# Kernel optimization log

Hardware: AMD Instinct MI355X
Metric: run time of the kernel (lower is better)

The kernel has to match this reference:

```python
import jax, jax.numpy as jnp
import numpy as np
from jax.scipy.special import logsumexp

D = 256; H = 8; A = D // H
B_CONST = 0.9; P_MAX = 50000.0; P_MIN = 1e-4; TANH_RATE = 0.005; EPS = 1e-10
SCALE = 1.0 / np.sqrt(D)


def setup_inputs() -> dict:
    key = jax.random.key(0)
    ks = jax.random.split(key, 5)
    B, S = 2, 512
    context = jax.random.normal(ks[0], (B, S, D), dtype=jnp.float32)
    W_Q = jax.random.normal(ks[1], (D, D), dtype=jnp.float32) * (1.0 / np.sqrt(D))
    W_KV = jax.random.normal(ks[2], (2 * D, D), dtype=jnp.float32) * (1.0 / np.sqrt(D))
    W_out = jax.random.normal(ks[3], (D, D), dtype=jnp.float32) * (1.0 / np.sqrt(D))
    p_param = jax.random.normal(ks[4], (D,), dtype=jnp.float32) * 0.02
    return {"context": context, "W_Q": W_Q, "W_KV": W_KV, "W_out": W_out, "p_param": p_param}


def reference(context, W_Q, W_KV, W_out, p_param):
    B, S, _ = context.shape
    # projections (nn.Linear: x @ W.T)
    q = context @ W_Q.T                          # [B,S,D]
    kv = context @ W_KV.T                        # [B,S,2D]
    k, v = kv[..., :D], kv[..., D:]
    # scaled p: p_max*tanh(tanh_rate*p)+1, then replace exact zeros with p_min
    p = P_MAX * jnp.tanh(TANH_RATE * p_param) + 1.0
    p = p + (p == 0).astype(p.dtype) * P_MIN
    # minmax-normalize v over the key/sequence axis into [b, 1]
    v_max = jnp.max(v, axis=-2, keepdims=True)   # [B,1,D]
    v_min = jnp.min(v, axis=-2, keepdims=True)
    v = (1.0 - B_CONST) * (v - v_min) / (v_max - v_min + EPS) + B_CONST
    z = p * jnp.log(v)                           # [B,S,D]
    # split heads
    qh = q.reshape(B, S, H, A).transpose(0, 2, 1, 3)          # [B,H,S,A]
    kh = k.reshape(B, S, H, A).transpose(0, 2, 1, 3)          # [B,H,S,A]
    zh = z.reshape(B, S, H, A).transpose(0, 2, 1, 3)[:, :, None]  # [B,H,1,K,A]
    dot = jnp.einsum('bhqa,bhka->bhqk', qh, kh)
    w = jax.nn.log_softmax(dot * SCALE, axis=-1)              # [B,H,Q,K]
    # log-domain power mean: logsumexp over keys of log-weights + p*log(v)
    mean = logsumexp(w[..., None] + zh, axis=-2)              # [B,H,Q,A]
    mean = mean.transpose(0, 2, 1, 3).reshape(B, S, D)
    e = jnp.exp(mean / p)
    # invert v minmax normalization
    e = (e - B_CONST) * (v_max - v_min + EPS) / (1.0 - B_CONST) + v_min
    return e @ W_out.T
```

## Files before the change

kernel.cpp:

```cpp
#include <hip/hip_runtime.h>
#include <math.h>

#define DD 256
#define HH 8
#define AA 32
#define SS 512
#define BB 2
constexpr float BCONST      = 0.9f;
constexpr float ONE_MINUS_B = 0.1f;
constexpr float EPSF        = 1e-10f;
constexpr float SCALEF      = 0.0625f;
constexpr float FLTMAX      = 3.402823466e38f;

#define OFF_QKV    0
#define OFF_VP     786432
#define OFF_EW     1048576
#define OFF_PMIN   1310720
#define OFF_PMAX   1318912
#define OFF_VMIN   1327104
#define OFF_VRANGE 1327616
#define OFF_P      1328128

#define KB4(buf, row, col4) \
  (&(buf)[((row) << 5) | ((((col4) >> 2) ^ (((row) >> 2) & 7)) << 2)])

template<int TM, int TN, int RM, int RN, bool MM>
__global__ __launch_bounds__(256) void gemm_t(
    const float* __restrict__ A, const float* __restrict__ B0,
    const float* __restrict__ B1, int nsplit,
    float* __restrict__ C, int ldc, int K, int lda,
    float* __restrict__ pminP, float* __restrict__ pmaxP) {
  constexpr int LDT = 36;
  constexpr int CG  = TN / RN;
  constexpr int NA  = TM * 32 / 1024;
  constexpr int NB  = TN * 32 / 1024;
  __shared__ float As[TM][LDT];
  __shared__ float Bs[TN][LDT];
  const int i0 = blockIdx.x * TM;
  const int j0 = blockIdx.y * TN;
  const float* Bsrc = (j0 < nsplit) ? (B0 + (size_t)j0 * K)
                                    : (B1 + (size_t)(j0 - nsplit) * K);
  const int t  = threadIdx.x;
  const int lr = t >> 3;
  const int lc = (t & 7) << 2;
  const int tx = t % CG, ty = t / CG;

  float4 pa[NA], pb[NB];
#pragma unroll
  for (int u = 0; u < NA; ++u)
    pa[u] = *(const float4*)(A + (size_t)(i0 + lr + 32 * u) * lda + lc);
#pragma unroll
  for (int u = 0; u < NB; ++u)
    pb[u] = *(const float4*)(Bsrc + (size_t)(lr + 32 * u) * K + lc);

  float acc[RM][RN] = {};
  for (int k0 = 0; k0 < K; k0 += 32) {
    __syncthreads();
#pragma unroll
    for (int u = 0; u < NA; ++u) *(float4*)&As[lr + 32 * u][lc] = pa[u];
#pragma unroll
    for (int u = 0; u < NB; ++u) *(float4*)&Bs[lr + 32 * u][lc] = pb[u];
    __syncthreads();
    if (k0 + 32 < K) {
#pragma unroll
      for (int u = 0; u < NA; ++u)
        pa[u] = *(const float4*)(A + (size_t)(i0 + lr + 32 * u) * lda + k0 + 32 + lc);
#pragma unroll
      for (int u = 0; u < NB; ++u)
        pb[u] = *(const float4*)(Bsrc + (size_t)(lr + 32 * u) * K + k0 + 32 + lc);
    }
#pragma unroll
    for (int kk = 0; kk < 32; kk += 4) {
      float4 af[RM], bf[RN];
#pragma unroll
      for (int r = 0; r < RM; ++r) af[r] = *(const float4*)&As[ty * RM + r][kk];
#pragma unroll
      for (int c = 0; c < RN; ++c) bf[c] = *(const float4*)&Bs[tx + CG * c][kk];
#pragma unroll
      for (int r = 0; r < RM; ++r)
#pragma unroll
        for (int c = 0; c < RN; ++c)
          acc[r][c] += af[r].x * bf[c].x + af[r].y * bf[c].y +
                       af[r].z * bf[c].z + af[r].w * bf[c].w;
    }
  }
#pragma unroll
  for (int r = 0; r < RM; ++r)
#pragma unroll
    for (int c = 0; c < RN; ++c)
      C[(size_t)(i0 + ty * RM + r) * ldc + j0 + tx + CG * c] = acc[r][c];

  if (MM && j0 >= 512) {
    __syncthreads();
    float* mnb = &As[0][0];
    float* mxb = &Bs[0][0];
#pragma unroll
    for (int c = 0; c < RN; ++c) {
      float mn = acc[0][c], mx = acc[0][c];
#pragma unroll
      for (int r = 1; r < RM; ++r) {
        mn = fminf(mn, acc[r][c]);
        mx = fmaxf(mx, acc[r][c]);
      }
      mnb[(tx + CG * c) * 17 + ty] = mn;
      mxb[(tx + CG * c) * 17 + ty] = mx;
    }
    __syncthreads();
    if (t < TN) {
      float mn = mnb[t * 17], mx = mxb[t * 17];
#pragma unroll
      for (int i = 1; i < 16; ++i) {
        mn = fminf(mn, mnb[t * 17 + i]);
        mx = fmaxf(mx, mxb[t * 17 + i]);
      }
      const int bx = i0 >> 5;
      pminP[bx * 256 + (j0 - 512) + t] = mn;
      pmaxP[bx * 256 + (j0 - 512) + t] = mx;
    }
  }
}

__global__ __launch_bounds__(256) void vpk(
    const float* __restrict__ qkv, const float* __restrict__ pminP,
    const float* __restrict__ pmaxP, const float* __restrict__ p_param,
    float* __restrict__ vp, float* __restrict__ vminw,
    float* __restrict__ vrangew, float* __restrict__ pw) {
  const int blk = blockIdx.x;
  const int b = blk >> 9, s = blk & 511;
  const int d = threadIdx.x;
  float mn = pminP[(b * 16) * 256 + d];
  float mx = pmaxP[(b * 16) * 256 + d];
#pragma unroll
  for (int c = 1; c < 16; ++c) {
    mn = fminf(mn, pminP[(b * 16 + c) * 256 + d]);
    mx = fmaxf(mx, pmaxP[(b * 16 + c) * 256 + d]);
  }
  float p = 50000.0f * tanhf(0.005f * p_param[d]) + 1.0f;
  if (p == 0.0f) p = 0.0001f;
  const float range = mx - mn + EPSF;
  const float v  = qkv[((size_t)(b * 512 + s)) * 768 + 512 + d];
  const float vn = (ONE_MINUS_B * (v - mn)) / range + BCONST;
  vp[(size_t)blk * 256 + d] = expm1f(p * logf(vn));
  if (s == 0) { vminw[b * 256 + d] = mn; vrangew[b * 256 + d] = range; }
  if (blk == 0) pw[d] = p;
}

__global__ __launch_bounds__(256) void attn_k(
    const float* __restrict__ qkv, const float* __restrict__ vp,
    const float* __restrict__ pw, const float* __restrict__ vminw,
    const float* __restrict__ vrangew, float* __restrict__ ew) {
  __shared__ float qs[32][36];
  __shared__ float sc[32 * 516];
  __shared__ float kb[512 * 32];
  __shared__ float red[32];
  const int bh  = blockIdx.y;
  const int b   = bh >> 3, h = bh & 7;
  const int q0g = blockIdx.x * 32;
  const int t   = threadIdx.x;
  const int srow = t >> 3, scol4 = (t & 7) << 2;

  {
    const int q = t >> 3, c4 = (t & 7) << 2;
    float4 qv = *(const float4*)(qkv + ((size_t)(b * 512 + q0g + q)) * 768 + h * 32 + c4);
    qv.x *= SCALEF; qv.y *= SCALEF; qv.z *= SCALEF; qv.w *= SCALEF;
    *(float4*)&qs[q][c4] = qv;
  }
#pragma unroll 8
  for (int u = 0; u < 16; ++u) {
    const int r = srow + 32 * u;
    float4 v = *(const float4*)(qkv + ((size_t)(b * 512 + r)) * 768 + 256 + h * 32 + scol4);
    *(float4*)KB4(kb, r, scol4) = v;
  }
  __syncthreads();

  {
    const int qgw = t >> 6;
    const int kg  = t & 63;
    float s8[8][8] = {};
#pragma unroll 2
    for (int kk = 0; kk < 32; kk += 4) {
      float4 qf[8], kf1[4], kf2[4];
#pragma unroll
      for (int r = 0; r < 8; ++r) qf[r] = *(const float4*)&qs[qgw + 4 * r][kk];
#pragma unroll
      for (int c = 0; c < 4; ++c) {
        kf1[c] = *(const float4*)KB4(kb, kg * 4 + c, kk);
        kf2[c] = *(const float4*)KB4(kb, 256 + kg * 4 + c, kk);
      }
#pragma unroll
      for (int r = 0; r < 8; ++r)
#pragma unroll
        for (int c = 0; c < 4; ++c) {
          s8[r][c]     += qf[r].x * kf1[c].x + qf[r].y * kf1[c].y +
                          qf[r].z * kf1[c].z + qf[r].w * kf1[c].w;
          s8[r][4 + c] += qf[r].x * kf2[c].x + qf[r].y * kf2[c].y +
                          qf[r].z * kf2[c].z + qf[r].w * kf2[c].w;
        }
    }
    float rs[8];
#pragma unroll
    for (int r = 0; r < 8; ++r) {
      float s = 0.f;
#pragma unroll
      for (int c = 0; c < 8; ++c) {
        s8[r][c] = __expf(s8[r][c]);
        s += s8[r][c];
      }
      rs[r] = s;
    }
#pragma unroll
    for (int m = 1; m < 64; m <<= 1)
#pragma unroll
      for (int r = 0; r < 8; ++r) rs[r] += __shfl_xor(rs[r], m);
    if ((t & 63) == 0)
#pragma unroll
      for (int r = 0; r < 8; ++r) red[qgw + 4 * r] = rs[r];
#pragma unroll
    for (int r = 0; r < 8; ++r) {
      const int rq = qgw + 4 * r;
      *(float4*)&sc[rq * 516 + kg * 4] =
          make_float4(s8[r][0], s8[r][1], s8[r][2], s8[r][3]);
      *(float4*)&sc[rq * 516 + 256 + kg * 4] =
          make_float4(s8[r][4], s8[r][5], s8[r][6], s8[r][7]);
    }
  }
  __syncthreads();

#pragma unroll 8
  for (int u = 0; u < 16; ++u) {
    const int r = srow + 32 * u;
    float4 v = *(const float4*)(vp + ((size_t)(b * 512 + r)) * 256 + h * 32 + scol4);
    *(float4*)KB4(kb, r, scol4) = v;
  }
  __syncthreads();

  const int ag  = t & 7;
  const int qg3 = (t >> 3) & 3;
  const int ks  = t >> 5;
  float a3[8][4] = {};
#pragma unroll 2
  for (int g = 0; g < 16; ++g) {
    const int kbase = ks * 64 + g * 4;
    float4 sq[8], vf[4];
#pragma unroll
    for (int r = 0; r < 8; ++r)
      sq[r] = *(const float4*)&sc[(qg3 + 4 * r) * 516 + kbase];
#pragma unroll
    for (int c = 0; c < 4; ++c)
      vf[c] = *(const float4*)KB4(kb, kbase + c, ag * 4);
#pragma unroll
    for (int r = 0; r < 8; ++r) {
      a3[r][0] += sq[r].x * vf[0].x + sq[r].y * vf[1].x + sq[r].z * vf[2].x + sq[r].w * vf[3].x;
      a3[r][1] += sq[r].x * vf[0].y + sq[r].y * vf[1].y + sq[r].z * vf[2].y + sq[r].w * vf[3].y;
      a3[r][2] += sq[r].x * vf[0].z + sq[r].y * vf[1].z + sq[r].z * vf[2].z + sq[r].w * vf[3].z;
      a3[r][3] += sq[r].x * vf[0].w + sq[r].y * vf[1].w + sq[r].z * vf[2].w + sq[r].w * vf[3].w;
    }
  }

#pragma unroll
  for (int r = 0; r < 8; ++r)
#pragma unroll
    for (int c = 0; c < 4; ++c)
      a3[r][c] += __shfl_xor(a3[r][c], 32);
  __syncthreads();
  float* part = &kb[0];
  if ((t & 32) == 0) {
    const int w = t >> 6;
#pragma unroll
    for (int r = 0; r < 8; ++r)
#pragma unroll
      for (int c = 0; c < 4; ++c)
        part[w * 1152 + (qg3 + 4 * r) * 36 + ag * 4 + c] = a3[r][c];
  }
  __syncthreads();

  {
    const int q = t >> 3, a0 = (t & 7) << 2;
    const int d0 = h * 32 + a0;
    const float invT = 1.0f / red[q];
    float4 s0 = *(const float4*)&part[q * 36 + a0];
    float4 s1 = *(const float4*)&part[1152 + q * 36 + a0];
    float4 s2 = *(const float4*)&part[2304 + q * 36 + a0];
    float4 s3 = *(const float4*)&part[3456 + q * 36 + a0];
    const float4 pp = *(const float4*)(pw + d0);
    const float4 vr = *(const float4*)(vrangew + b * 256 + d0);
    const float4 vm = *(const float4*)(vminw + b * 256 + d0);
    float4 o;
    o.x = (expf(log1pf((s0.x + s1.x + s2.x + s3.x) * invT) / pp.x) - BCONST) * vr.x / ONE_MINUS_B + vm.x;
    o.y = (expf(log1pf((s0.y + s1.y + s2.y + s3.y) * invT) / pp.y) - BCONST) * vr.y / ONE_MINUS_B + vm.y;
    o.z = (expf(log1pf((s0.z + s1.z + s2.z + s3.z) * invT) / pp.z) - BCONST) * vr.z / ONE_MINUS_B + vm.z;
    o.w = (expf(log1pf((s0.w + s1.w + s2.w + s3.w) * invT) / pp.w) - BCONST) * vr.w / ONE_MINUS_B + vm.w;
    *(float4*)(ew + ((size_t)(b * 512 + q0g + q)) * 256 + d0) = o;
  }
}

extern "C" void kernel_launch(void* const* d_in, const int* in_sizes, int n_in,
                              void* d_out, int out_size, void* d_ws, size_t ws_size,
                              hipStream_t stream) {
  const float* ctx  = (const float*)d_in[0];
  const float* WQ   = (const float*)d_in[1];
  const float* WKV  = (const float*)d_in[2];
  const float* WOUT = (const float*)d_in[3];
  const float* PP   = (const float*)d_in[4];
  float* ws      = (float*)d_ws;
  float* qkv     = ws + OFF_QKV;
  float* vp      = ws + OFF_VP;
  float* ew      = ws + OFF_EW;
  float* pminP   = ws + OFF_PMIN;
  float* pmaxP   = ws + OFF_PMAX;
  float* vminw   = ws + OFF_VMIN;
  float* vrangew = ws + OFF_VRANGE;
  float* pw      = ws + OFF_P;
  float* out     = (float*)d_out;

  gemm_t<32, 64, 2, 4, true><<<dim3(32, 12), 256, 0, stream>>>(
      ctx, WQ, WKV, 256, qkv, 768, 256, 256, pminP, pmaxP);
  vpk<<<1024, 256, 0, stream>>>(qkv, pminP, pmaxP, PP, vp, vminw, vrangew, pw);
  attn_k<<<dim3(16, 16), 256, 0, stream>>>(qkv, vp, pw, vminw, vrangew, ew);
  gemm_t<32, 32, 2, 2, false><<<dim3(32, 8), 256, 0, stream>>>(
      ew, WOUT, WOUT, 1 << 30, out, 256, 256, 256, nullptr, nullptr);
}
```

Baseline: 107.8 us.

## Fuse vp, attention and output GEMM into one persistent kernel with grid barriers

Merges the three kernels that follow the QKV projection (v power transform, attention, output projection) into one 256-block kernel. A hand-rolled atomic-counter grid barrier separates the stages, and a memset resets the counters on every call. This removes two kernel launch gaps and tail effects. In exchange it adds a memset launch and spin-wait barriers, and it depends on all 256 blocks being co-resident, which the large shared-memory footprint and single-block-per-CU launch bound could threaten.

```diff
diff --git a/kernel.cpp b/kernel.cpp
--- a/kernel.cpp
+++ b/kernel.cpp
@@ -20,20 +20,31 @@
 #define OFF_VMIN   1327104
 #define OFF_VRANGE 1327616
 #define OFF_P      1328128
+#define OFF_CTR    1328384
 
 #define KB4(buf, row, col4) \
   (&(buf)[((row) << 5) | ((((col4) >> 2) ^ (((row) >> 2) & 7)) << 2)])
 
-template<int TM, int TN, int RM, int RN, bool MM>
-__global__ __launch_bounds__(256) void gemm_t(
+__device__ __forceinline__ void gbar(unsigned int* c, unsigned int tgt) {
+  __syncthreads();
+  if (threadIdx.x == 0) {
+    __threadfence();
+    atomicAdd(c, 1u);
+    while (atomicAdd(c, 0u) < tgt) __builtin_amdgcn_s_sleep(4);
+    __threadfence();
+  }
+  __syncthreads();
+}
+
+__global__ __launch_bounds__(256) void gemm_qkv(
     const float* __restrict__ A, const float* __restrict__ B0,
     const float* __restrict__ B1, int nsplit,
     float* __restrict__ C, int ldc, int K, int lda,
     float* __restrict__ pminP, float* __restrict__ pmaxP) {
+  constexpr int TM = 32, TN = 64, RM = 2, RN = 4;
   constexpr int LDT = 36;
   constexpr int CG  = TN / RN;
-  constexpr int NA  = TM * 32 / 1024;
-  constexpr int NB  = TN * 32 / 1024;
+  constexpr int NA  = 1, NB = 2;
   __shared__ float As[TM][LDT];
   __shared__ float Bs[TN][LDT];
   const int i0 = blockIdx.x * TM;
@@ -90,7 +101,7 @@
     for (int c = 0; c < RN; ++c)
       C[(size_t)(i0 + ty * RM + r) * ldc + j0 + tx + CG * c] = acc[r][c];
 
-  if (MM && j0 >= 512) {
+  if (j0 >= 512) {
     __syncthreads();
     float* mnb = &As[0][0];
     float* mxb = &Bs[0][0];
@@ -120,177 +131,230 @@
   }
 }
 
-__global__ __launch_bounds__(256) void vpk(
+__global__ __launch_bounds__(256, 1) void mega(
     const float* __restrict__ qkv, const float* __restrict__ pminP,
     const float* __restrict__ pmaxP, const float* __restrict__ p_param,
     float* __restrict__ vp, float* __restrict__ vminw,
-    float* __restrict__ vrangew, float* __restrict__ pw) {
-  const int blk = blockIdx.x;
-  const int b = blk >> 9, s = blk & 511;
-  const int d = threadIdx.x;
-  float mn = pminP[(b * 16) * 256 + d];
-  float mx = pmaxP[(b * 16) * 256 + d];
-#pragma unroll
-  for (int c = 1; c < 16; ++c) {
-    mn = fminf(mn, pminP[(b * 16 + c) * 256 + d]);
-    mx = fmaxf(mx, pmaxP[(b * 16 + c) * 256 + d]);
-  }
-  float p = 50000.0f * tanhf(0.005f * p_param[d]) + 1.0f;
-  if (p == 0.0f) p = 0.0001f;
-  const float range = mx - mn + EPSF;
-  const float v  = qkv[((size_t)(b * 512 + s)) * 768 + 512 + d];
-  const float vn = (ONE_MINUS_B * (v - mn)) / range + BCONST;
-  vp[(size_t)blk * 256 + d] = expm1f(p * logf(vn));
-  if (s == 0) { vminw[b * 256 + d] = mn; vrangew[b * 256 + d] = range; }
-  if (blk == 0) pw[d] = p;
-}
-
-__global__ __launch_bounds__(256) void attn_k(
-    const float* __restrict__ qkv, const float* __restrict__ vp,
-    const float* __restrict__ pw, const float* __restrict__ vminw,
-    const float* __restrict__ vrangew, float* __restrict__ ew) {
+    float* __restrict__ vrangew, float* __restrict__ pw,
+    float* __restrict__ ew, const float* __restrict__ WOUT,
+    float* __restrict__ out, unsigned int* __restrict__ ctr) {
   __shared__ float qs[32][36];
   __shared__ float sc[32 * 516];
   __shared__ float kb[512 * 32];
   __shared__ float red[32];
-  const int bh  = blockIdx.y;
-  const int b   = bh >> 3, h = bh & 7;
-  const int q0g = blockIdx.x * 32;
+  const int bid = blockIdx.x;
   const int t   = threadIdx.x;
-  const int srow = t >> 3, scol4 = (t & 7) << 2;
 
   {
-    const int q = t >> 3, c4 = (t & 7) << 2;
-    float4 qv = *(const float4*)(qkv + ((size_t)(b * 512 + q0g + q)) * 768 + h * 32 + c4);
-    qv.x *= SCALEF; qv.y *= SCALEF; qv.z *= SCALEF; qv.w *= SCALEF;
-    *(float4*)&qs[q][c4] = qv;
-  }
+    const int u0 = bid * 4;
+    const int b  = u0 >> 9;
+    const int d  = t;
+    float mn = pminP[(b * 16) * 256 + d];
+    float mx = pmaxP[(b * 16) * 256 + d];
+#pragma unroll
+    for (int c = 1; c < 16; ++c) {
+      mn = fminf(mn, pminP[(b * 16 + c) * 256 + d]);
+      mx = fmaxf(mx, pmaxP[(b * 16 + c) * 256 + d]);
+    }
+    float p = 50000.0f * tanhf(0.005f * p_param[d]) + 1.0f;
+    if (p == 0.0f) p = 0.0001f;
+    const float range = mx - mn + EPSF;
+#pragma unroll
+    for (int i = 0; i < 4; ++i) {
+      const float v  = qkv[((size_t)(u0 + i)) * 768 + 512 + d];
+      const float vn = (ONE_MINUS_B * (v - mn)) / range + BCONST;
+      vp[(size_t)(u0 + i) * 256 + d] = expm1f(p * logf(vn));
+    }
+    if ((bid & 127) == 0) {
+      vminw[b * 256 + d] = mn;
+      vrangew[b * 256 + d] = range;
+    }
+    if (bid == 0) pw[d] = p;
+  }
+  gbar(ctr + 0, 256u);
+
+  {
+    const int q0g = (bid & 15) * 32;
+    const int bh  = bid >> 4;
+    const int b   = bh >> 3, h = bh & 7;
+    const int srow = t >> 3, scol4 = (t & 7) << 2;
+
+    {
+      const int q = t >> 3, c4 = (t & 7) << 2;
+      float4 qv = *(const float4*)(qkv + ((size_t)(b * 512 + q0g + q)) * 768 + h * 32 + c4);
+      qv.x *= SCALEF; qv.y *= SCALEF; qv.z *= SCALEF; qv.w *= SCALEF;
+      *(float4*)&qs[q][c4] = qv;
+    }
 #pragma unroll 8
-  for (int u = 0; u < 16; ++u) {
-    const int r = srow + 32 * u;
-    float4 v = *(const float4*)(qkv + ((size_t)(b * 512 + r)) * 768 + 256 + h * 32 + scol4);
-    *(float4*)KB4(kb, r, scol4) = v;
-  }
-  __syncthreads();
+    for (int u = 0; u < 16; ++u) {
+      const int r = srow + 32 * u;
+      float4 v = *(const float4*)(qkv + ((size_t)(b * 512 + r)) * 768 + 256 + h * 32 + scol4);
+      *(float4*)KB4(kb, r, scol4) = v;
+    }
+    __syncthreads();
+
+    {
+      const int qgw = t >> 6;
+      const int kg  = t & 63;
+      float s8[8][8] = {};
+#pragma unroll 2
+      for (int kk = 0; kk < 32; kk += 4) {
+        float4 qf[8], kf1[4], kf2[4];
+#pragma unroll
+        for (int r = 0; r < 8; ++r) qf[r] = *(const float4*)&qs[qgw + 4 * r][kk];
+#pragma unroll
+        for (int c = 0; c < 4; ++c) {
+          kf1[c] = *(const float4*)KB4(kb, kg * 4 + c, kk);
+          kf2[c] = *(const float4*)KB4(kb, 256 + kg * 4 + c, kk);
+        }
+#pragma unroll
+        for (int r = 0; r < 8; ++r)
+#pragma unroll
+          for (int c = 0; c < 4; ++c) {
+            s8[r][c]     += qf[r].x * kf1[c].x + qf[r].y * kf1[c].y +
+                            qf[r].z * kf1[c].z + qf[r].w * kf1[c].w;
+            s8[r][4 + c] += qf[r].x * kf2[c].x + qf[r].y * kf2[c].y +
+                            qf[r].z * kf2[c].z + qf[r].w * kf2[c].w;
+          }
+      }
+      float rs[8];
+#pragma unroll
+      for (int r = 0; r < 8; ++r) {
+        float s = 0.f;
+#pragma unroll
+        for (int c = 0; c < 8; ++c) {
+          s8[r][c] = __expf(s8[r][c]);
+          s += s8[r][c];
+        }
+        rs[r] = s;
+      }
+#pragma unroll
+      for (int m = 1; m < 64; m <<= 1)
+#pragma unroll
+        for (int r = 0; r < 8; ++r) rs[r] += __shfl_xor(rs[r], m);
+      if ((t & 63) == 0)
+#pragma unroll
+        for (int r = 0; r < 8; ++r) red[qgw + 4 * r] = rs[r];
+#pragma unroll
+      for (int r = 0; r < 8; ++r) {
+        const int rq = qgw + 4 * r;
+        *(float4*)&sc[rq * 516 + kg * 4] =
+            make_float4(s8[r][0], s8[r][1], s8[r][2], s8[r][3]);
+        *(float4*)&sc[rq * 516 + 256 + kg * 4] =
+            make_float4(s8[r][4], s8[r][5], s8[r][6], s8[r][7]);
+      }
+    }
+    __syncthreads();
+
+#pragma unroll 8
+    for (int u = 0; u < 16; ++u) {
+      const int r = srow + 32 * u;
+      float4 v = *(const float4*)(vp + ((size_t)(b * 512 + r)) * 256 + h * 32 + scol4);
+      *(float4*)KB4(kb, r, scol4) = v;
+    }
+    __syncthreads();
+
+    const int ag  = t & 7;
+    const int qg3 = (t >> 3) & 3;
+    const int ks  = t >> 5;
+    float a3[8][4] = {};
+#pragma unroll 2
+    for (int g = 0; g < 16; ++g) {
+      const int kbase = ks * 64 + g * 4;
+      float4 sq[8], vf[4];
+#pragma unroll
+      for (int r = 0; r < 8; ++r)
+        sq[r] = *(const float4*)&sc[(qg3 + 4 * r) * 516 + kbase];
+#pragma unroll
+      for (int c = 0; c < 4; ++c)
+        vf[c] = *(const float4*)KB4(kb, kbase + c, ag * 4);
+#pragma unroll
+      for (int r = 0; r < 8; ++r) {
+        a3[r][0] += sq[r].x * vf[0].x + sq[r].y * vf[1].x + sq[r].z * vf[2].x + sq[r].w * vf[3].x;
+        a3[r][1] += sq[r].x * vf[0].y + sq[r].y * vf[1].y + sq[r].z * vf[2].y + sq[r].w * vf[3].y;
+        a3[r][2] += sq[r].x * vf[0].z + sq[r].y * vf[1].z + sq[r].z * vf[2].z + sq[r].w * vf[3].z;
+        a3[r][3] += sq[r].x * vf[0].w + sq[r].y * vf[1].w + sq[r].z * vf[2].w + sq[r].w * vf[3].w;
+      }
+    }
+#pragma unroll
+    for (int r = 0; r < 8; ++r)
+#pragma unroll
+      for (int c = 0; c < 4; ++c)
+        a3[r][c] += __shfl_xor(a3[r][c], 32);
+    __syncthreads();
+    float* part = &kb[0];
+    if ((t & 32) == 0) {
+      const int w = t >> 6;
+#pragma unroll
+      for (int r = 0; r < 8; ++r)
+#pragma unroll
+        for (int c = 0; c < 4; ++c)
+          part[w * 1152 + (qg3 + 4 * r) * 36 + ag * 4 + c] = a3[r][c];
+    }
+    __syncthreads();
+    {
+      const int q = t >> 3, a0 = (t & 7) << 2;
+      const int d0 = h * 32 + a0;
+      const float invT = 1.0f / red[q];
+      float4 s0 = *(const float4*)&part[q * 36 + a0];
+      float4 s1 = *(const float4*)&part[1152 + q * 36 + a0];
+      float4 s2 = *(const float4*)&part[2304 + q * 36 + a0];
+      float4 s3 = *(const float4*)&part[3456 + q * 36 + a0];
+      const float4 pp = *(const float4*)(pw + d0);
+      const float4 vr = *(const float4*)(vrangew + b * 256 + d0);
+      const float4 vm = *(const float4*)(vminw + b * 256 + d0);
+      float4 o;
+      o.x = (expf(log1pf((s0.x + s1.x + s2.x + s3.x) * invT) / pp.x) - BCONST) * vr.x / ONE_MINUS_B + vm.x;
+      o.y = (expf(log1pf((s0.y + s1.y + s2.y + s3.y) * invT) / pp.y) - BCONST) * vr.y / ONE_MINUS_B + vm.y;
+      o.z = (expf(log1pf((s0.z + s1.z + s2.z + s3.z) * invT) / pp.z) - BCONST) * vr.z / ONE_MINUS_B + vm.z;
+      o.w = (expf(log1pf((s0.w + s1.w + s2.w + s3.w) * invT) / pp.w) - BCONST) * vr.w / ONE_MINUS_B + vm.w;
+      *(float4*)(ew + ((size_t)(b * 512 + q0g + q)) * 256 + d0) = o;
+    }
+  }
+  gbar(ctr + 1, 256u);
 
   {
-    const int qgw = t >> 6;
-    const int kg  = t & 63;
-    float s8[8][8] = {};
-#pragma unroll 2
-    for (int kk = 0; kk < 32; kk += 4) {
-      float4 qf[8], kf1[4], kf2[4];
-#pragma unroll
-      for (int r = 0; r < 8; ++r) qf[r] = *(const float4*)&qs[qgw + 4 * r][kk];
-#pragma unroll
-      for (int c = 0; c < 4; ++c) {
-        kf1[c] = *(const float4*)KB4(kb, kg * 4 + c, kk);
-        kf2[c] = *(const float4*)KB4(kb, 256 + kg * 4 + c, kk);
-      }
-#pragma unroll
-      for (int r = 0; r < 8; ++r)
-#pragma unroll
-        for (int c = 0; c < 4; ++c) {
-          s8[r][c]     += qf[r].x * kf1[c].x + qf[r].y * kf1[c].y +
-                          qf[r].z * kf1[c].z + qf[r].w * kf1[c].w;
-          s8[r][4 + c] += qf[r].x * kf2[c].x + qf[r].y * kf2[c].y +
-                          qf[r].z * kf2[c].z + qf[r].w * kf2[c].w;
-        }
-    }
-    float rs[8];
-#pragma unroll
-    for (int r = 0; r < 8; ++r) {
-      float s = 0.f;
-#pragma unroll
-      for (int c = 0; c < 8; ++c) {
-        s8[r][c] = __expf(s8[r][c]);
-        s += s8[r][c];
-      }
-      rs[r] = s;
-    }
-#pragma unroll
-    for (int m = 1; m < 64; m <<= 1)
-#pragma unroll
-      for (int r = 0; r < 8; ++r) rs[r] += __shfl_xor(rs[r], m);
-    if ((t & 63) == 0)
-#pragma unroll
-      for (int r = 0; r < 8; ++r) red[qgw + 4 * r] = rs[r];
-#pragma unroll
-    for (int r = 0; r < 8; ++r) {
-      const int rq = qgw + 4 * r;
-      *(float4*)&sc[rq * 516 + kg * 4] =
-          make_float4(s8[r][0], s8[r][1], s8[r][2], s8[r][3]);
-      *(float4*)&sc[rq * 516 + 256 + kg * 4] =
-          make_float4(s8[r][4], s8[r][5], s8[r][6], s8[r][7]);
-    }
-  }
-  __syncthreads();
-
-#pragma unroll 8
-  for (int u = 0; u < 16; ++u) {
-    const int r = srow + 32 * u;
-    float4 v = *(const float4*)(vp + ((size_t)(b * 512 + r)) * 256 + h * 32 + scol4);
-    *(float4*)KB4(kb, r, scol4) = v;
-  }
-  __syncthreads();
-
-  const int ag  = t & 7;
-  const int qg3 = (t >> 3) & 3;
-  const int ks  = t >> 5;
-  float a3[8][4] = {};
-#pragma unroll 2
-  for (int g = 0; g < 16; ++g) {
-    const int kbase = ks * 64 + g * 4;
-    float4 sq[8], vf[4];
-#pragma unroll
-    for (int r = 0; r < 8; ++r)
-      sq[r] = *(const float4*)&sc[(qg3 + 4 * r) * 516 + kbase];
-#pragma unroll
-    for (int c = 0; c < 4; ++c)
-      vf[c] = *(const float4*)KB4(kb, kbase + c, ag * 4);
-#pragma unroll
-    for (int r = 0; r < 8; ++r) {
-      a3[r][0] += sq[r].x * vf[0].x + sq[r].y * vf[1].x + sq[r].z * vf[2].x + sq[r].w * vf[3].x;
-      a3[r][1] += sq[r].x * vf[0].y + sq[r].y * vf[1].y + sq[r].z * vf[2].y + sq[r].w * vf[3].y;
-      a3[r][2] += sq[r].x * vf[0].z + sq[r].y * vf[1].z + sq[r].z * vf[2].z + sq[r].w * vf[3].z;
-      a3[r][3] += sq[r].x * vf[0].w + sq[r].y * vf[1].w + sq[r].z * vf[2].w + sq[r].w * vf[3].w;
-    }
-  }
-
-#pragma unroll
-  for (int r = 0; r < 8; ++r)
-#pragma unroll
-    for (int c = 0; c < 4; ++c)
-      a3[r][c] += __shfl_xor(a3[r][c], 32);
-  __syncthreads();
-  float* part = &kb[0];
-  if ((t & 32) == 0) {
-    const int w = t >> 6;
-#pragma unroll
-    for (int r = 0; r < 8; ++r)
-#pragma unroll
-      for (int c = 0; c < 4; ++c)
-        part[w * 1152 + (qg3 + 4 * r) * 36 + ag * 4 + c] = a3[r][c];
-  }
-  __syncthreads();
-
-  {
-    const int q = t >> 3, a0 = (t & 7) << 2;
-    const int d0 = h * 32 + a0;
-    const float invT = 1.0f / red[q];
-    float4 s0 = *(const float4*)&part[q * 36 + a0];
-    float4 s1 = *(const float4*)&part[1152 + q * 36 + a0];
-    float4 s2 = *(const float4*)&part[2304 + q * 36 + a0];
-    float4 s3 = *(const float4*)&part[3456 + q * 36 + a0];
-    const float4 pp = *(const float4*)(pw + d0);
-    const float4 vr = *(const float4*)(vrangew + b * 256 + d0);
-    const float4 vm = *(const float4*)(vminw + b * 256 + d0);
-    float4 o;
-    o.x = (expf(log1pf((s0.x + s1.x + s2.x + s3.x) * invT) / pp.x) - BCONST) * vr.x / ONE_MINUS_B + vm.x;
-    o.y = (expf(log1pf((s0.y + s1.y + s2.y + s3.y) * invT) / pp.y) - BCONST) * vr.y / ONE_MINUS_B + vm.y;
-    o.z = (expf(log1pf((s0.z + s1.z + s2.z + s3.z) * invT) / pp.z) - BCONST) * vr.z / ONE_MINUS_B + vm.z;
-    o.w = (expf(log1pf((s0.w + s1.w + s2.w + s3.w) * invT) / pp.w) - BCONST) * vr.w / ONE_MINUS_B + vm.w;
-    *(float4*)(ew + ((size_t)(b * 512 + q0g + q)) * 256 + d0) = o;
+    float (*As)[36] = qs;
+    float (*Bs)[36] = (float(*)[36])&sc[0];
+    const int i0 = (bid & 31) * 32;
+    const int j0 = (bid >> 5) * 32;
+    const int lr = t >> 3;
+    const int lc = (t & 7) << 2;
+    const int tx = t & 15, ty = t >> 4;
+    const float* Bsrc = WOUT + (size_t)j0 * 256;
+
+    float4 pa = *(const float4*)(ew + (size_t)(i0 + lr) * 256 + lc);
+    float4 pb = *(const float4*)(Bsrc + (size_t)lr * 256 + lc);
+    float acc[2][2] = {};
+    for (int k0 = 0; k0 < 256; k0 += 32) {
+      __syncthreads();
+      *(float4*)&As[lr][lc] = pa;
+      *(float4*)&Bs[lr][lc] = pb;
+      __syncthreads();
+      if (k0 + 32 < 256) {
+        pa = *(const float4*)(ew + (size_t)(i0 + lr) * 256 + k0 + 32 + lc);
+        pb = *(const float4*)(Bsrc + (size_t)lr * 256 + k0 + 32 + lc);
+      }
+#pragma unroll
+      for (int kk = 0; kk < 32; kk += 4) {
+        float4 af[2], bf[2];
+#pragma unroll
+        for (int r = 0; r < 2; ++r) af[r] = *(const float4*)&As[ty * 2 + r][kk];
+#pragma unroll
+        for (int c = 0; c < 2; ++c) bf[c] = *(const float4*)&Bs[tx + 16 * c][kk];
+#pragma unroll
+        for (int r = 0; r < 2; ++r)
+#pragma unroll
+          for (int c = 0; c < 2; ++c)
+            acc[r][c] += af[r].x * bf[c].x + af[r].y * bf[c].y +
+                         af[r].z * bf[c].z + af[r].w * bf[c].w;
+      }
+    }
+#pragma unroll
+    for (int r = 0; r < 2; ++r)
+#pragma unroll
+      for (int c = 0; c < 2; ++c)
+        out[(size_t)(i0 + ty * 2 + r) * 256 + j0 + tx + 16 * c] = acc[r][c];
   }
 }
 
@@ -311,12 +375,14 @@
   float* vminw   = ws + OFF_VMIN;
   float* vrangew = ws + OFF_VRANGE;
   float* pw      = ws + OFF_P;
+  unsigned int* ctr = (unsigned int*)(ws + OFF_CTR);
   float* out     = (float*)d_out;
 
-  gemm_t<32, 64, 2, 4, true><<<dim3(32, 12), 256, 0, stream>>>(
+  hipMemsetAsync(ctr, 0, 2 * sizeof(unsigned int), stream);
+
+  gemm_qkv<<<dim3(32, 12), 256, 0, stream>>>(
       ctx, WQ, WKV, 256, qkv, 768, 256, 256, pminP, pmaxP);
-  vpk<<<1024, 256, 0, stream>>>(qkv, pminP, pmaxP, PP, vp, vminw, vrangew, pw);
-  attn_k<<<dim3(16, 16), 256, 0, stream>>>(qkv, vp, pw, vminw, vrangew, ew);
-  gemm_t<32, 32, 2, 2, false><<<dim3(32, 8), 256, 0, stream>>>(
-      ew, WOUT, WOUT, 1 << 30, out, 256, 256, 256, nullptr, nullptr);
+
+  mega<<<256, 256, 0, stream>>>(
+      qkv, pminP, pmaxP, PP, vp, vminw, vrangew, pw, ew, WOUT, out, ctr);
 }
```

New measurement: 140.6 us. +30.4%, slower.
